# Kernel optimization log

Measured on AMD Instinct MI355X. Metric: run time of the kernel, lower is better.

The kernel has to match this reference:

```python
import jax, jax.numpy as jnp
import numpy as np

V, E, H, L, B, T = 50257, 1024, 16, 8, 2, 2048
HD = E // H  # head_dim = 64
FF = 4 * E
EPS = 1e-5


def setup_inputs() -> dict:
    key = jax.random.key(0)
    ks = jax.random.split(key, 12)
    s = 0.02  # init std as in _init_weights
    return {
        "idx": jax.random.randint(ks[0], (B, T), 0, V, dtype=jnp.int64) if jax.config.jax_enable_x64 else jax.random.randint(ks[0], (B, T), 0, V, dtype=jnp.int32),
        "targets": jax.random.randint(ks[1], (B, T), 0, V, dtype=jnp.int32),
        "wte": jax.random.normal(ks[2], (V, E), jnp.float32) * s,
        "wpe": jax.random.normal(ks[3], (T, E), jnp.float32) * s,
        "qkv_w": jax.random.normal(ks[4], (L, E, 3 * E), jnp.float32) * s,
        "proj_w": jax.random.normal(ks[5], (L, E, E), jnp.float32) * s,
        "proj_b": jnp.zeros((L, E), jnp.float32),
        "ln1_g": jnp.ones((L, E), jnp.float32),
        "ln1_b": jnp.zeros((L, E), jnp.float32),
        "ln2_g": jnp.ones((L, E), jnp.float32),
        "ln2_b": jnp.zeros((L, E), jnp.float32),
        "fc1_w": jax.random.normal(ks[6], (L, E, FF), jnp.float32) * s,
        "fc1_b": jnp.zeros((L, FF), jnp.float32),
        "fc2_w": jax.random.normal(ks[7], (L, FF, E), jnp.float32) * s,
        "fc2_b": jnp.zeros((L, E), jnp.float32),
        "lnf_g": jnp.ones((E,), jnp.float32),
        "lnf_b": jnp.zeros((E,), jnp.float32),
    }


def _layer_norm(x, g, b):
    mean = x.mean(-1, keepdims=True)
    var = ((x - mean) ** 2).mean(-1, keepdims=True)  # unbiased=False
    return g * (x - mean) / jnp.sqrt(var + EPS) + b


def _gpt_forward(idx, targets, wte, wpe, qkv_w, proj_w, proj_b,
                 ln1_g, ln1_b, ln2_g, ln2_b, fc1_w, fc1_b, fc2_w, fc2_b,
                 lnf_g, lnf_b):
    Bq, Tq = idx.shape
    x = wte[idx] + wpe[:Tq][None, :, :]  # [B,T,E]
    causal = jnp.tril(jnp.ones((Tq, Tq), bool))  # [T,T]
    scale = 1.0 / np.sqrt(HD)

    def block(x, p):
        (qw, pw, pb, g1, b1, g2, b2, f1w, f1b, f2w, f2b) = p
        h = _layer_norm(x, g1, b1)
        qkv = h @ qw  # [B,T,3E]
        qkv = qkv.reshape(Bq, Tq, 3, H, HD).transpose(2, 0, 3, 1, 4)  # [3,B,H,T,HD]
        q, k, v = qkv[0], qkv[1], qkv[2]
        att = jnp.einsum('bhqd,bhkd->bhqk', q, k) * scale
        att = jnp.where(causal[None, None], att, -jnp.inf)
        att = jax.nn.softmax(att, axis=-1)  # dropout=0.0 -> identity
        y = jnp.einsum('bhqk,bhkd->bhqd', att, v)
        y = y.transpose(0, 2, 1, 3).reshape(Bq, Tq, E)
        x = x + y @ pw + pb
        h = _layer_norm(x, g2, b2)
        h = jax.nn.gelu(h @ f1w + f1b, approximate=False)  # torch nn.GELU = exact erf
        x = x + h @ f2w + f2b
        return x, None

    params = (qkv_w, proj_w, proj_b, ln1_g, ln1_b, ln2_g, ln2_b,
              fc1_w, fc1_b, fc2_w, fc2_b)
    x, _ = jax.lax.scan(block, x, params)
    x = _layer_norm(x, lnf_g, lnf_b)
    logits = x @ wte.T  # tied lm_head, [B,T,V]
    logp = jax.nn.log_softmax(logits, axis=-1)
    nll = -jnp.take_along_axis(logp, targets[..., None], axis=-1)[..., 0]
    loss = nll.mean()
    return logits, loss


def reference(idx, targets, wte, wpe, qkv_w, proj_w, proj_b,
              ln1_g, ln1_b, ln2_g, ln2_b, fc1_w, fc1_b, fc2_w, fc2_b,
              lnf_g, lnf_b):
    return _gpt_forward(idx, targets, wte, wpe, qkv_w, proj_w, proj_b,
                        ln1_g, ln1_b, ln2_g, ln2_b, fc1_w, fc1_b, fc2_w, fc2_b,
                        lnf_g, lnf_b)
```

## Files before the change

### kernel.cpp

```cpp
#include <hip/hip_runtime.h>
#include <math.h>

constexpr int Vv = 50257;
constexpr int Ee = 1024;
constexpr int Hh = 16;
constexpr int Ll = 8;
constexpr int Bb = 2;
constexpr int Tt = 2048;
constexpr int HDh = 64;
constexpr int FFf = 4096;
constexpr int BT = Bb * Tt;

typedef __attribute__((ext_vector_type(8))) short bf16x8;
typedef __attribute__((ext_vector_type(4))) float f32x4;

__device__ __forceinline__ short f2b(float f) {
    union { float f; unsigned u; } c; c.f = f;
    unsigned u = c.u + 0x7fffu + ((c.u >> 16) & 1u);
    return (short)(u >> 16);
}

__device__ __forceinline__ void g2l16(void* lds, const void* g) {
    __builtin_amdgcn_global_load_lds(
        (const __attribute__((address_space(1))) void*)g,
        (__attribute__((address_space(3))) void*)lds, 16, 0, 0);
}

__device__ __forceinline__ float gelu_exact(float v) {
    return 0.5f * v * (1.0f + erff(v * 0.70710678118654752f));
}

__global__ __launch_bounds__(256) void k_embed(const int* __restrict__ idx,
                                               const float* __restrict__ wte,
                                               const float* __restrict__ wpe,
                                               float* __restrict__ x) {
    const int row = blockIdx.x;
    const int t = row % Tt;
    const int tok = idx[row];
    const int c = threadIdx.x * 4;
    const float4 a = *(const float4*)(wte + (size_t)tok * Ee + c);
    const float4 b = *(const float4*)(wpe + (size_t)t * Ee + c);
    *(float4*)(x + (size_t)row * Ee + c) =
        make_float4(a.x + b.x, a.y + b.y, a.z + b.z, a.w + b.w);
}

__global__ __launch_bounds__(256) void k_ln(const float* __restrict__ x,
                                            const float* __restrict__ g,
                                            const float* __restrict__ b,
                                            short* __restrict__ out) {
    const int row = blockIdx.x;
    const int tid = threadIdx.x;
    const float4 v = *(const float4*)(x + (size_t)row * Ee + tid * 4);
    float s  = v.x + v.y + v.z + v.w;
    float ss = v.x * v.x + v.y * v.y + v.z * v.z + v.w * v.w;
#pragma unroll
    for (int off = 32; off; off >>= 1) {
        s  += __shfl_down(s, off);
        ss += __shfl_down(ss, off);
    }
    __shared__ float red[8];
    const int wid = tid >> 6, lane = tid & 63;
    if (lane == 0) { red[wid] = s; red[4 + wid] = ss; }
    __syncthreads();
    const float S  = red[0] + red[1] + red[2] + red[3];
    const float SS = red[4] + red[5] + red[6] + red[7];
    const float mean = S * (1.f / Ee);
    const float var  = SS * (1.f / Ee) - mean * mean;
    const float inv  = rsqrtf(var + 1e-5f);
    const float4 gg = *(const float4*)(g + tid * 4);
    const float4 bb = *(const float4*)(b + tid * 4);
    short4 o;
    o.x = f2b((v.x - mean) * inv * gg.x + bb.x);
    o.y = f2b((v.y - mean) * inv * gg.y + bb.y);
    o.z = f2b((v.z - mean) * inv * gg.z + bb.z);
    o.w = f2b((v.w - mean) * inv * gg.w + bb.w);
    *(short4*)(out + (size_t)row * Ee + tid * 4) = o;
}

__global__ __launch_bounds__(256) void k_wT(const float* __restrict__ w,
                                            short* __restrict__ o, int K, int N) {
    __shared__ short t[32][33];
    const int n0 = blockIdx.x * 32, k0 = blockIdx.y * 32;
    const int tid = threadIdx.x;
    {
        const int k = tid >> 3, n4 = (tid & 7) * 4;
        const float4 v = *(const float4*)(w + (size_t)(k0 + k) * N + n0 + n4);
        t[n4 + 0][k] = f2b(v.x); t[n4 + 1][k] = f2b(v.y);
        t[n4 + 2][k] = f2b(v.z); t[n4 + 3][k] = f2b(v.w);
    }
    __syncthreads();
    {
        const int n = tid >> 3, k4 = (tid & 7) * 4;
        short4 s;
        s.x = t[n][k4]; s.y = t[n][k4 + 1]; s.z = t[n][k4 + 2]; s.w = t[n][k4 + 3];
        *(short4*)(o + (size_t)(n0 + n) * K + k0 + k4) = s;
    }
}

__global__ __launch_bounds__(256) void k_cvt(const float* __restrict__ w,
                                             short* __restrict__ o, int n8) {
    const int i = blockIdx.x * 256 + threadIdx.x;
    if (i >= n8) return;
    const float4 a = ((const float4*)w)[i * 2];
    const float4 b = ((const float4*)w)[i * 2 + 1];
    bf16x8 v = {f2b(a.x), f2b(a.y), f2b(a.z), f2b(a.w),
                f2b(b.x), f2b(b.y), f2b(b.z), f2b(b.w)};
    ((bf16x8*)o)[i] = v;
}

__device__ __forceinline__ void st_c(float* C, size_t i, float v) { C[i] = v; }
__device__ __forceinline__ void st_c(short* C, size_t i, float v) { C[i] = f2b(v); }

template <int EPI, int SWZ, int BN64f, int WAVES, typename OT>
__global__ __launch_bounds__(WAVES * 64) void k_gemm(const short* __restrict__ A,
                                              const short* __restrict__ Bp,
                                              const float* __restrict__ bias,
                                              const float* __restrict__ res,
                                              OT* __restrict__ C,
                                              int M, int N, int K,
                                              float* __restrict__ pmax,
                                              float* __restrict__ psum) {
    constexpr int BM = (WAVES / 2) * 64;
    constexpr int BN = BN64f ? 64 : 128;
    constexpr int NJ = BN64f ? 2 : 4;
    constexpr int WCOL = BN64f ? 32 : 64;
    __shared__ short As[BM * 32];
    __shared__ short Bs[BN * 32];
    const int tid = threadIdx.x, w = tid >> 6, ln = tid & 63;
    int bx = blockIdx.x, by = blockIdx.y;
    if (SWZ) {
        const int nwg = gridDim.x * gridDim.y;
        const int orig = by * gridDim.x + bx;
        const int q = nwg >> 3, r = nwg & 7;
        const int xcd = orig & 7, local = orig >> 3;
        const int wgid = (xcd < r ? xcd * (q + 1) : r * (q + 1) + (xcd - r) * q) + local;
        if (SWZ == 1) { bx = wgid % gridDim.x; by = wgid / gridDim.x; }
        else          { bx = wgid / gridDim.y; by = wgid % gridDim.y; }
    }
    const int m0 = bx * BM, n0 = by * BN;
    const int wr = w >> 1, wc = w & 1;

    f32x4 zero = {0.f, 0.f, 0.f, 0.f};
    f32x4 acc[4][NJ];
#pragma unroll
    for (int i = 0; i < 4; i++)
#pragma unroll
        for (int j = 0; j < NJ; j++) acc[i][j] = zero;

    const int srow = w * 32 + (ln >> 2);
    const int scol = (ln & 3) * 8;
    const int sb   = tid >> 2;
    const int sb8  = w * 16 + (ln >> 2);
    const int br0 = min(n0 + srow, N - 1);
    const int br1 = min(n0 + srow + 16, N - 1);
    const int brs = min(n0 + sb, N - 1);
    const int br8 = min(n0 + sb8, N - 1);

    for (int k0 = 0; k0 < K; k0 += 32) {
        __syncthreads();
        g2l16(&As[(w * 32 + 0) * 32],  A + (size_t)(m0 + srow) * K + k0 + scol);
        g2l16(&As[(w * 32 + 16) * 32], A + (size_t)(m0 + srow + 16) * K + k0 + scol);
        if (BN64f) {
            g2l16(&Bs[sb * 32], Bp + (size_t)brs * K + k0 + scol);
        } else if (WAVES == 8) {
            g2l16(&Bs[(w * 16) * 32], Bp + (size_t)br8 * K + k0 + scol);
        } else {
            g2l16(&Bs[(w * 32 + 0) * 32],  Bp + (size_t)br0 * K + k0 + scol);
            g2l16(&Bs[(w * 32 + 16) * 32], Bp + (size_t)br1 * K + k0 + scol);
        }
        __syncthreads();
        bf16x8 af[4], bfv[NJ];
#pragma unroll
        for (int i = 0; i < 4; i++)
            af[i]  = *(bf16x8*)&As[(wr * 64 + i * 16 + (ln & 15)) * 32 + (ln >> 4) * 8];
#pragma unroll
        for (int j = 0; j < NJ; j++)
            bfv[j] = *(bf16x8*)&Bs[(wc * WCOL + j * 16 + (ln & 15)) * 32 + (ln >> 4) * 8];
#pragma unroll
        for (int i = 0; i < 4; i++)
#pragma unroll
            for (int j = 0; j < NJ; j++)
                acc[i][j] = __builtin_amdgcn_mfma_f32_16x16x32_bf16(
                    af[i], bfv[j], acc[i][j], 0, 0, 0);
    }

#pragma unroll
    for (int j = 0; j < NJ; j++) {
        const int gcol = n0 + wc * WCOL + j * 16 + (ln & 15);
        if (gcol < N) {
            const float bv = (EPI == 2 || EPI == 3) ? bias[gcol] : 0.f;
#pragma unroll
            for (int i = 0; i < 4; i++) {
#pragma unroll
                for (int r = 0; r < 4; r++) {
                    const int grow = m0 + wr * 64 + i * 16 + (ln >> 4) * 4 + r;
                    float v = acc[i][j][r] + bv;
                    if (EPI == 2) v = gelu_exact(v);
                    if (EPI == 3) v += res[(size_t)grow * N + gcol];
                    st_c(C, (size_t)grow * N + gcol, v);
                }
            }
        }
    }
    if (EPI == 4) {
        const size_t slot = (size_t)(by * 2 + wc) * M;
#pragma unroll
        for (int i = 0; i < 4; i++) {
#pragma unroll
            for (int r = 0; r < 4; r++) {
                const int grow = m0 + wr * 64 + i * 16 + (ln >> 4) * 4 + r;
                float vv[NJ], pm = -INFINITY;
#pragma unroll
                for (int j = 0; j < NJ; j++) {
                    const int gcol = n0 + wc * WCOL + j * 16 + (ln & 15);
                    vv[j] = (gcol < N) ? acc[i][j][r] : -INFINITY;
                    pm = fmaxf(pm, vv[j]);
                }
#pragma unroll
                for (int off = 1; off < 16; off <<= 1) pm = fmaxf(pm, __shfl_xor(pm, off));
                float ps = 0.f;
#pragma unroll
                for (int j = 0; j < NJ; j++)
                    ps += (vv[j] > -INFINITY) ? __expf(vv[j] - pm) : 0.f;
#pragma unroll
                for (int off = 1; off < 16; off <<= 1) ps += __shfl_xor(ps, off);
                if ((ln & 15) == 0) {
                    pmax[slot + grow] = pm;
                    psum[slot + grow] = ps;
                }
            }
        }
    }
}

__global__ __launch_bounds__(256) void k_attn(const short* __restrict__ qkv,
                                              short* __restrict__ y) {
    __shared__ short Kl[64][72];
    __shared__ short Vt[64][72];
    __shared__ short Pl[4][16][72];
    const int tid = threadIdx.x, w = tid >> 6, ln = tid & 63;
    const int lo = blockIdx.x;
    const int hi = (Tt / 64 - 1) - lo;
    const int h = blockIdx.y, b = blockIdx.z;
    const size_t base = ((size_t)b * Tt) * (3 * Ee) + h * HDh;
    const int q0s[2] = {lo * 64, hi * 64};

    bf16x8 qf[2][2];
#pragma unroll
    for (int s = 0; s < 2; s++) {
        const int qr = q0s[s] + w * 16 + (ln & 15);
        const short* qp = qkv + base + (size_t)qr * (3 * Ee) + (ln >> 4) * 8;
        qf[s][0] = *(const bf16x8*)(qp);
        qf[s][1] = *(const bf16x8*)(qp + 32);
    }

    f32x4 zero = {0.f, 0.f, 0.f, 0.f};
    f32x4 oc[2][4];
#pragma unroll
    for (int s = 0; s < 2; s++)
#pragma unroll
        for (int i = 0; i < 4; i++) oc[s][i] = zero;
    float mx[2][4], ls[2][4];
#pragma unroll
    for (int s = 0; s < 2; s++)
#pragma unroll
        for (int r = 0; r < 4; r++) { mx[s][r] = -INFINITY; ls[s][r] = 0.f; }

    const int nt = hi + 1;
    for (int j = 0; j < nt; j++) {
        const int kb = j * 64;
        __syncthreads();
        {
            const int r = tid >> 2, d0 = (tid & 3) * 16;
            const short* kp = qkv + base + Ee     + (size_t)(kb + r) * (3 * Ee) + d0;
            const short* vp = qkv + base + 2 * Ee + (size_t)(kb + r) * (3 * Ee) + d0;
            *(bf16x8*)&Kl[r][d0]     = *(const bf16x8*)(kp);
            *(bf16x8*)&Kl[r][d0 + 8] = *(const bf16x8*)(kp + 8);
            bf16x8 v0 = *(const bf16x8*)(vp);
            bf16x8 v1 = *(const bf16x8*)(vp + 8);
#pragma unroll
            for (int p = 0; p < 8; p++) Vt[d0 + p][r] = v0[p];
#pragma unroll
            for (int p = 0; p < 8; p++) Vt[d0 + 8 + p][r] = v1[p];
        }
        __syncthreads();

#pragma unroll
        for (int s = 1; s >= 0; s--) {
            if (s == 0 && j > lo) continue;
            f32x4 sc[4];
#pragma unroll
            for (int kcb = 0; kcb < 4; kcb++) {
                const int krow = kcb * 16 + (ln & 15);
                bf16x8 kf0 = *(bf16x8*)&Kl[krow][(ln >> 4) * 8];
                bf16x8 kf1 = *(bf16x8*)&Kl[krow][(ln >> 4) * 8 + 32];
                f32x4 ss = __builtin_amdgcn_mfma_f32_16x16x32_bf16(qf[s][0], kf0, zero, 0, 0, 0);
                sc[kcb]  = __builtin_amdgcn_mfma_f32_16x16x32_bf16(qf[s][1], kf1, ss, 0, 0, 0);
            }
            float pv[4][4];
            float tmv[4] = {-INFINITY, -INFINITY, -INFINITY, -INFINITY};
#pragma unroll
            for (int kcb = 0; kcb < 4; kcb++) {
                const int col = kb + kcb * 16 + (ln & 15);
#pragma unroll
                for (int r = 0; r < 4; r++) {
                    const int qr = q0s[s] + w * 16 + (ln >> 4) * 4 + r;
                    const float sv = (col <= qr) ? sc[kcb][r] * 0.125f : -INFINITY;
                    pv[kcb][r] = sv;
                    tmv[r] = fmaxf(tmv[r], sv);
                }
            }
#pragma unroll
            for (int off = 1; off < 16; off <<= 1)
#pragma unroll
                for (int r = 0; r < 4; r++) tmv[r] = fmaxf(tmv[r], __shfl_xor(tmv[r], off));
            float rs[4];
#pragma unroll
            for (int r = 0; r < 4; r++) {
                const float nm = fmaxf(mx[s][r], tmv[r]);
                const float alpha = __expf(mx[s][r] - nm);
                mx[s][r] = nm;
                float acc_s = 0.f;
#pragma unroll
                for (int kcb = 0; kcb < 4; kcb++) {
                    const float e = __expf(pv[kcb][r] - nm);
                    pv[kcb][r] = e;
                    acc_s += e;
                }
                rs[r] = acc_s;
                ls[s][r] *= alpha;
#pragma unroll
                for (int db = 0; db < 4; db++) oc[s][db][r] *= alpha;
            }
#pragma unroll
            for (int off = 1; off < 16; off <<= 1)
#pragma unroll
                for (int r = 0; r < 4; r++) rs[r] += __shfl_xor(rs[r], off);
#pragma unroll
            for (int r = 0; r < 4; r++) ls[s][r] += rs[r];
#pragma unroll
            for (int kcb = 0; kcb < 4; kcb++)
#pragma unroll
                for (int r = 0; r < 4; r++)
                    Pl[w][(ln >> 4) * 4 + r][kcb * 16 + (ln & 15)] = f2b(pv[kcb][r]);
            bf16x8 pf0 = *(bf16x8*)&Pl[w][ln & 15][(ln >> 4) * 8];
            bf16x8 pf1 = *(bf16x8*)&Pl[w][ln & 15][(ln >> 4) * 8 + 32];
#pragma unroll
            for (int db = 0; db < 4; db++) {
                const int drow = db * 16 + (ln & 15);
                bf16x8 vf0 = *(bf16x8*)&Vt[drow][(ln >> 4) * 8];
                bf16x8 vf1 = *(bf16x8*)&Vt[drow][(ln >> 4) * 8 + 32];
                oc[s][db] = __builtin_amdgcn_mfma_f32_16x16x32_bf16(pf0, vf0, oc[s][db], 0, 0, 0);
                oc[s][db] = __builtin_amdgcn_mfma_f32_16x16x32_bf16(pf1, vf1, oc[s][db], 0, 0, 0);
            }
        }
    }
#pragma unroll
    for (int s = 0; s < 2; s++)
#pragma unroll
        for (int r = 0; r < 4; r++) {
            const int qr = q0s[s] + w * 16 + (ln >> 4) * 4 + r;
            const float inv = 1.f / ls[s][r];
#pragma unroll
            for (int db = 0; db < 4; db++)
                y[(size_t)(b * Tt + qr) * Ee + h * HDh + db * 16 + (ln & 15)] =
                    f2b(oc[s][db][r] * inv);
        }
}

__global__ __launch_bounds__(256) void k_loss_fin(const float* __restrict__ pmax,
                                                  const float* __restrict__ psum,
                                                  const float* __restrict__ logits,
                                                  const int* __restrict__ targets,
                                                  float* __restrict__ rnll, int nt2) {
    const int row = blockIdx.x * 256 + threadIdx.x;
    float M = -INFINITY, S = 0.f;
    for (int i = 0; i < nt2; i++) {
        const float pm = pmax[(size_t)i * BT + row];
        const float ps = psum[(size_t)i * BT + row];
        const float nm = fmaxf(M, pm);
        S = S * __expf(M - nm) + ps * __expf(pm - nm);
        M = nm;
    }
    rnll[row] = (M + logf(S)) - logits[(size_t)row * Vv + targets[row]];
}

__global__ __launch_bounds__(256) void k_loss_final(const float* __restrict__ rnll,
                                                    float* __restrict__ loss) {
    const int tid = threadIdx.x;
    float s = 0.f;
    for (int i = tid; i < BT; i += 256) s += rnll[i];
#pragma unroll
    for (int off = 32; off; off >>= 1) s += __shfl_xor(s, off);
    __shared__ float red[4];
    if ((tid & 63) == 0) red[tid >> 6] = s;
    __syncthreads();
    if (tid == 0) loss[0] = (red[0] + red[1] + red[2] + red[3]) / (float)BT;
}

extern "C" void kernel_launch(void* const* d_in, const int* in_sizes, int n_in,
                              void* d_out, int out_size, void* d_ws, size_t ws_size,
                              hipStream_t stream) {
    const int*   idx     = (const int*)d_in[0];
    const int*   targets = (const int*)d_in[1];
    const float* wte     = (const float*)d_in[2];
    const float* wpe     = (const float*)d_in[3];
    const float* qkv_w   = (const float*)d_in[4];
    const float* proj_w  = (const float*)d_in[5];
    const float* proj_b  = (const float*)d_in[6];
    const float* ln1_g   = (const float*)d_in[7];
    const float* ln1_b   = (const float*)d_in[8];
    const float* ln2_g   = (const float*)d_in[9];
    const float* ln2_b   = (const float*)d_in[10];
    const float* fc1_w   = (const float*)d_in[11];
    const float* fc1_b   = (const float*)d_in[12];
    const float* fc2_w   = (const float*)d_in[13];
    const float* fc2_b   = (const float*)d_in[14];
    const float* lnf_g   = (const float*)d_in[15];
    const float* lnf_b   = (const float*)d_in[16];

    float* logits = (float*)d_out;
    float* loss   = logits + (size_t)BT * Vv;

    constexpr int NT2 = 2 * ((Vv + 127) / 128);

    short* wteb = (short*)d_ws;
    float* x    = (float*)d_ws;
    short* qkvb = (short*)(x + (size_t)BT * Ee);
    short* y    = qkvb + (size_t)BT * 3 * Ee;
    short* h1   = y + (size_t)BT * Ee;
    short* wT   = h1 + (size_t)BT * FFf;
    const size_t OFF = (size_t)Vv * Ee * 2;
    short* h    = (short*)((char*)d_ws + OFF);
    float* rnll = (float*)(h + (size_t)BT * Ee);
    float* pmax = rnll + BT;
    float* psum = pmax + (size_t)BT * NT2;
    const size_t need = OFF + (size_t)BT * Ee * 2
                      + (BT + 2 * (size_t)BT * NT2) * sizeof(float);
    if (ws_size < need) return;

    k_embed<<<BT, 256, 0, stream>>>(idx, wte, wpe, x);
    for (int l = 0; l < Ll; l++) {
        k_ln<<<BT, 256, 0, stream>>>(x, ln1_g + (size_t)l * Ee, ln1_b + (size_t)l * Ee, h);
        k_wT<<<dim3(3 * Ee / 32, Ee / 32), 256, 0, stream>>>(
            qkv_w + (size_t)l * Ee * 3 * Ee, wT, Ee, 3 * Ee);
        k_gemm<0, 1, 0, 4, short><<<dim3(BT / 128, 3 * Ee / 128), 256, 0, stream>>>(
            h, wT, nullptr, nullptr, qkvb, BT, 3 * Ee, Ee, nullptr, nullptr);
        k_attn<<<dim3(Tt / 128, Hh, Bb), 256, 0, stream>>>(qkvb, y);
        k_wT<<<dim3(Ee / 32, Ee / 32), 256, 0, stream>>>(
            proj_w + (size_t)l * Ee * Ee, wT, Ee, Ee);
        k_gemm<3, 1, 1, 4, float><<<dim3(BT / 128, Ee / 64), 256, 0, stream>>>(
            y, wT, proj_b + (size_t)l * Ee, x, x, BT, Ee, Ee, nullptr, nullptr);
        k_ln<<<BT, 256, 0, stream>>>(x, ln2_g + (size_t)l * Ee, ln2_b + (size_t)l * Ee, h);
        k_wT<<<dim3(FFf / 32, Ee / 32), 256, 0, stream>>>(
            fc1_w + (size_t)l * Ee * FFf, wT, Ee, FFf);
        k_gemm<2, 1, 0, 4, short><<<dim3(BT / 128, FFf / 128), 256, 0, stream>>>(
            h, wT, fc1_b + (size_t)l * FFf, nullptr, h1, BT, FFf, Ee, nullptr, nullptr);
        k_wT<<<dim3(Ee / 32, FFf / 32), 256, 0, stream>>>(
            fc2_w + (size_t)l * FFf * Ee, wT, FFf, Ee);
        k_gemm<3, 1, 1, 4, float><<<dim3(BT / 128, Ee / 64), 256, 0, stream>>>(
            h1, wT, fc2_b + (size_t)l * Ee, x, x, BT, Ee, FFf, nullptr, nullptr);
    }
    k_ln<<<BT, 256, 0, stream>>>(x, lnf_g, lnf_b, h);
    k_cvt<<<(Vv * Ee / 8 + 255) / 256, 256, 0, stream>>>(wte, wteb, Vv * Ee / 8);
    k_gemm<4, 2, 0, 8, float><<<dim3(BT / 256, (Vv + 127) / 128), 512, 0, stream>>>(
        h, wteb, nullptr, nullptr, logits, BT, Vv, Ee, pmax, psum);
    k_loss_fin<<<BT / 256, 256, 0, stream>>>(pmax, psum, logits, targets, rnll, NT2);
    k_loss_final<<<1, 256, 0, stream>>>(rnll, loss);
}
```

Baseline: 3.837 ms.

## Pre-transpose V into a separate buffer and use 8-wave GEMM tiles for QKV/FC1

Adds a k_vT kernel that transposes the V slice of the QKV output into a [E, BT] buffer once per layer. The attention kernel can then load V tiles with vectorized row loads instead of scattering element-wise transposed stores into LDS on every key block. The QKV and FC1 GEMMs also switch to the 8-wave, 512-thread configuration with 256-row tiles. The cost is one extra kernel launch and an extra read and write of V per layer, plus a new workspace region placed after wT.

```diff
diff --git a/kernel.cpp b/kernel.cpp
--- a/kernel.cpp
+++ b/kernel.cpp
@@ -94,6 +94,27 @@
         short4 s;
         s.x = t[n][k4]; s.y = t[n][k4 + 1]; s.z = t[n][k4 + 2]; s.w = t[n][k4 + 3];
         *(short4*)(o + (size_t)(n0 + n) * K + k0 + k4) = s;
+    }
+}
+
+__global__ __launch_bounds__(256) void k_vT(const short* __restrict__ qkv,
+                                            short* __restrict__ vT) {
+    __shared__ short t[32][33];
+    const int r0 = blockIdx.x * 32;
+    const int c0 = blockIdx.y * 32;
+    const int tid = threadIdx.x;
+    {
+        const int r = tid >> 3, c4 = (tid & 7) * 4;
+        const short4 v = *(const short4*)(qkv + (size_t)(r0 + r) * (3 * Ee) + 2 * Ee + c0 + c4);
+        t[c4 + 0][r] = v.x; t[c4 + 1][r] = v.y;
+        t[c4 + 2][r] = v.z; t[c4 + 3][r] = v.w;
+    }
+    __syncthreads();
+    {
+        const int c = tid >> 3, r4 = (tid & 7) * 4;
+        short4 s;
+        s.x = t[c][r4]; s.y = t[c][r4 + 1]; s.z = t[c][r4 + 2]; s.w = t[c][r4 + 3];
+        *(short4*)(vT + (size_t)(c0 + c) * BT + r0 + r4) = s;
     }
 }
 
@@ -234,6 +255,7 @@
 }
 
 __global__ __launch_bounds__(256) void k_attn(const short* __restrict__ qkv,
+                                              const short* __restrict__ vT,
                                               short* __restrict__ y) {
     __shared__ short Kl[64][72];
     __shared__ short Vt[64][72];
@@ -272,16 +294,12 @@
         __syncthreads();
         {
             const int r = tid >> 2, d0 = (tid & 3) * 16;
-            const short* kp = qkv + base + Ee     + (size_t)(kb + r) * (3 * Ee) + d0;
-            const short* vp = qkv + base + 2 * Ee + (size_t)(kb + r) * (3 * Ee) + d0;
+            const short* kp = qkv + base + Ee + (size_t)(kb + r) * (3 * Ee) + d0;
             *(bf16x8*)&Kl[r][d0]     = *(const bf16x8*)(kp);
             *(bf16x8*)&Kl[r][d0 + 8] = *(const bf16x8*)(kp + 8);
-            bf16x8 v0 = *(const bf16x8*)(vp);
-            bf16x8 v1 = *(const bf16x8*)(vp + 8);
-#pragma unroll
-            for (int p = 0; p < 8; p++) Vt[d0 + p][r] = v0[p];
-#pragma unroll
-            for (int p = 0; p < 8; p++) Vt[d0 + 8 + p][r] = v1[p];
+            const short* vp = vT + (size_t)(h * HDh + r) * BT + (size_t)b * Tt + kb + d0;
+            *(bf16x8*)&Vt[r][d0]     = *(const bf16x8*)(vp);
+            *(bf16x8*)&Vt[r][d0 + 8] = *(const bf16x8*)(vp + 8);
         }
         __syncthreads();
 
@@ -430,6 +448,7 @@
     short* y    = qkvb + (size_t)BT * 3 * Ee;
     short* h1   = y + (size_t)BT * Ee;
     short* wT   = h1 + (size_t)BT * FFf;
+    short* vT   = wT + (size_t)FFf * Ee;
     const size_t OFF = (size_t)Vv * Ee * 2;
     short* h    = (short*)((char*)d_ws + OFF);
     float* rnll = (float*)(h + (size_t)BT * Ee);
@@ -444,9 +463,10 @@
         k_ln<<<BT, 256, 0, stream>>>(x, ln1_g + (size_t)l * Ee, ln1_b + (size_t)l * Ee, h);
         k_wT<<<dim3(3 * Ee / 32, Ee / 32), 256, 0, stream>>>(
             qkv_w + (size_t)l * Ee * 3 * Ee, wT, Ee, 3 * Ee);
-        k_gemm<0, 1, 0, 4, short><<<dim3(BT / 128, 3 * Ee / 128), 256, 0, stream>>>(
+        k_gemm<0, 1, 0, 8, short><<<dim3(BT / 256, 3 * Ee / 128), 512, 0, stream>>>(
             h, wT, nullptr, nullptr, qkvb, BT, 3 * Ee, Ee, nullptr, nullptr);
-        k_attn<<<dim3(Tt / 128, Hh, Bb), 256, 0, stream>>>(qkvb, y);
+        k_vT<<<dim3(BT / 32, Ee / 32), 256, 0, stream>>>(qkvb, vT);
+        k_attn<<<dim3(Tt / 128, Hh, Bb), 256, 0, stream>>>(qkvb, vT, y);
         k_wT<<<dim3(Ee / 32, Ee / 32), 256, 0, stream>>>(
             proj_w + (size_t)l * Ee * Ee, wT, Ee, Ee);
         k_gemm<3, 1, 1, 4, float><<<dim3(BT / 128, Ee / 64), 256, 0, stream>>>(
@@ -454,7 +474,7 @@
         k_ln<<<BT, 256, 0, stream>>>(x, ln2_g + (size_t)l * Ee, ln2_b + (size_t)l * Ee, h);
         k_wT<<<dim3(FFf / 32, Ee / 32), 256, 0, stream>>>(
             fc1_w + (size_t)l * Ee * FFf, wT, Ee, FFf);
-        k_gemm<2, 1, 0, 4, short><<<dim3(BT / 128, FFf / 128), 256, 0, stream>>>(
+        k_gemm<2, 1, 0, 8, short><<<dim3(BT / 256, FFf / 128), 512, 0, stream>>>(
             h, wT, fc1_b + (size_t)l * FFf, nullptr, h1, BT, FFf, Ee, nullptr, nullptr);
         k_wT<<<dim3(Ee / 32, FFf / 32), 256, 0, stream>>>(
             fc2_w + (size_t)l * FFf * Ee, wT, FFf, Ee);
```

New measurement: 3.648 ms. 1.05x faster.
